# Kernel tuning notes

Measured on AMD Instinct MI355X. Metric: run time of the kernel, lower is better.

The kernel has to match this reference:

```python
import jax, jax.numpy as jnp
from jax import lax
import numpy as np

K, D, BETA = 512, 64, 0.25

def conv1d(x, w, b=None, stride=1, padding=0):
    # x: [N,C,L], w: [O,I,k] (torch layout)
    y = lax.conv_general_dilated(x, w, (stride,), [(padding, padding)],
                                 dimension_numbers=('NCH', 'OIH', 'NCH'))
    return y if b is None else y + b[None, :, None]

def conv_transpose1d(x, w, b, stride, padding):
    # torch ConvTranspose1d; w: [I,O,k]. Equivalent to dilated conv with flipped, transposed kernel.
    k = w.shape[2]
    wf = jnp.flip(w, 2).transpose(1, 0, 2)  # [O,I,k]
    y = lax.conv_general_dilated(x, wf, (1,), [(k - 1 - padding, k - 1 - padding)],
                                 lhs_dilation=(stride,),
                                 dimension_numbers=('NCH', 'OIH', 'NCH'))
    return y + b[None, :, None]

def residual_stack(x, blocks):
    for w1, w2 in blocks:
        h = conv1d(jax.nn.relu(x), w1, None, 1, 1)
        h = conv1d(jax.nn.relu(h), w2, None, 1, 0)
        x = x + h
    return jax.nn.relu(x)

def setup_inputs() -> dict:
    key = jax.random.key(0)
    ks = iter(jax.random.split(key, 32))
    def w(shape, fan_in):
        return jax.random.normal(next(ks), shape, jnp.float32) / np.sqrt(fan_in)
    H, RH = 128, 32
    inp = {
        'x': jax.random.normal(next(ks), (64, 1, 8192), jnp.float32),
        'ec1_w': w((H // 2, 1, 4), 4), 'ec1_b': jnp.zeros(H // 2, jnp.float32),
        'ec2_w': w((H, H // 2, 4), H // 2 * 4), 'ec2_b': jnp.zeros(H, jnp.float32),
        'ec3_w': w((H, H, 3), H * 3), 'ec3_b': jnp.zeros(H, jnp.float32),
        'er1_w1': w((RH, H, 3), H * 3), 'er1_w2': w((H, RH, 1), RH),
        'er2_w1': w((RH, H, 3), H * 3), 'er2_w2': w((H, RH, 1), RH),
        'pvq_w': w((D, H, 1), H), 'pvq_b': jnp.zeros(D, jnp.float32),
        'codebook': jax.random.uniform(next(ks), (K, D), jnp.float32, -1.0 / K, 1.0 / K),
        'dc1_w': w((H, D, 3), D * 3), 'dc1_b': jnp.zeros(H, jnp.float32),
        'dr1_w1': w((RH, H, 3), H * 3), 'dr1_w2': w((H, RH, 1), RH),
        'dr2_w1': w((RH, H, 3), H * 3), 'dr2_w2': w((H, RH, 1), RH),
        'dt1_w': w((H, H // 2, 4), H * 4), 'dt1_b': jnp.zeros(H // 2, jnp.float32),
        'dt2_w': w((H // 2, 1, 4), H // 2 * 4), 'dt2_b': jnp.zeros(1, jnp.float32),
    }
    return inp

def reference(x, ec1_w, ec1_b, ec2_w, ec2_b, ec3_w, ec3_b,
              er1_w1, er1_w2, er2_w1, er2_w2, pvq_w, pvq_b, codebook,
              dc1_w, dc1_b, dr1_w1, dr1_w2, dr2_w1, dr2_w2,
              dt1_w, dt1_b, dt2_w, dt2_b):
    # ---- Encoder (compression_factor == 4) ----
    h = jax.nn.relu(conv1d(x, ec1_w, ec1_b, 2, 1))
    h = jax.nn.relu(conv1d(h, ec2_w, ec2_b, 2, 1))
    h = conv1d(h, ec3_w, ec3_b, 1, 1)
    h = residual_stack(h, [(er1_w1, er1_w2), (er2_w1, er2_w2)])
    z = conv1d(h, pvq_w, pvq_b, 1, 0)            # [B, D, L/4]

    # ---- Vector quantizer ----
    z_blc = z.transpose(0, 2, 1)                 # [B, L', D]
    flat = z_blc.reshape(-1, D)                  # [N, D]
    dists = (jnp.sum(flat * flat, 1, keepdims=True)
             - 2.0 * flat @ codebook.T
             + jnp.sum(codebook * codebook, 1))  # [N, K]
    idx = jnp.argmin(dists, axis=1)              # [N]
    q = codebook[idx].reshape(z_blc.shape)       # [B, L', D]
    e_latent = jnp.mean((lax.stop_gradient(q) - z_blc) ** 2)
    q_latent = jnp.mean((q - lax.stop_gradient(z_blc)) ** 2)
    vq_loss = q_latent + BETA * e_latent
    q_st = z_blc + lax.stop_gradient(q - z_blc)  # straight-through
    counts = jnp.zeros((K,), z.dtype).at[idx].add(1.0)
    avg_probs = counts / idx.shape[0]
    perplexity = jnp.exp(-jnp.sum(avg_probs * jnp.log(avg_probs + 1e-10)))

    # ---- Decoder (compression_factor == 4) ----
    d = conv1d(q_st.transpose(0, 2, 1), dc1_w, dc1_b, 1, 1)
    d = residual_stack(d, [(dr1_w1, dr1_w2), (dr2_w1, dr2_w2)])
    d = jax.nn.relu(conv_transpose1d(d, dt1_w, dt1_b, 2, 1))
    recon = conv_transpose1d(d, dt2_w, dt2_b, 2, 1)  # [B, 1, L]
    return recon, vq_loss, perplexity
```

## Files before the change

### kernel.cpp

```cpp
#include <hip/hip_runtime.h>
#include <math.h>

static constexpr int NB  = 64;
static constexpr int L0  = 8192;
static constexpr int L1  = 4096;
static constexpr int LQ  = 2048;
static constexpr int CH  = 128;
static constexpr int CHH = 64;
static constexpr int CR  = 32;
static constexpr int CD  = 64;
static constexpr int NK  = 512;
static constexpr int NROWS = NB * LQ;

using short8 = __attribute__((ext_vector_type(8))) short;
using f32x4  = __attribute__((ext_vector_type(4))) float;

__device__ inline f32x4 mfma16(short8 a, short8 b, f32x4 c) {
    return __builtin_amdgcn_mfma_f32_16x16x32_bf16(a, b, c, 0, 0, 0);
}

__device__ inline unsigned short bf16rne(float v) {
    unsigned int bb = __builtin_bit_cast(unsigned int, v);
    unsigned int r = (bb + 0x7FFFu + ((bb >> 16) & 1u)) >> 16;
    return (unsigned short)r;
}
__device__ inline float bf2f(unsigned short s) {
    unsigned int u = ((unsigned int)s) << 16;
    return __builtin_bit_cast(float, u);
}

__global__ __launch_bounds__(256) void k_wtf(const float* __restrict__ src,
                                             short* __restrict__ dst,
                                             int CO, int CI, int K, int iok) {
    int i = blockIdx.x * 256 + threadIdx.x;
    int total = K * CO * CI;
    if (i >= total) return;
    int j  = i & 7;
    int hi = (i >> 3) & 3;
    int cl = (i >> 5) & 15;
    int rest = i >> 9;
    int CIb = CI >> 5, COb = CO >> 4;
    int kb = rest % CIb; rest /= CIb;
    int cb = rest % COb;
    int tap = rest / COb;
    int co = cb * 16 + cl, ci = kb * 32 + hi * 8 + j;
    float v = iok ? src[(ci * CO + co) * K + tap] : src[(co * CI + ci) * K + tap];
    dst[i] = (short)bf16rne(v);
}

__global__ __launch_bounds__(256) void k_w2f(const float* __restrict__ src,
                                             short* __restrict__ hi_dst,
                                             short* __restrict__ lo_dst) {
    int i = blockIdx.x * 256 + threadIdx.x;
    if (i >= CH * CR) return;
    int j  = i & 7;
    int hi = (i >> 3) & 3;
    int cl = (i >> 5) & 15;
    int cb = i >> 9;
    int co = cb * 16 + cl, ci = hi * 8 + j;
    float v = src[co * CR + ci];
    unsigned short h = bf16rne(v);
    hi_dst[i] = (short)h;
    lo_dst[i] = (short)bf16rne(v - bf2f(h));
}

__global__ __launch_bounds__(256) void k_pwf(const float* __restrict__ src,
                                             short* __restrict__ hi_dst,
                                             short* __restrict__ lo_dst) {
    int i = blockIdx.x * 256 + threadIdx.x;
    if (i >= CD * CH) return;
    int j  = i & 7;
    int hi = (i >> 3) & 3;
    int cl = (i >> 5) & 15;
    int rest = i >> 9;
    int kb = rest & 3, cb = rest >> 2;
    int d = cb * 16 + cl, ci = kb * 32 + hi * 8 + j;
    float v = src[d * CH + ci];
    unsigned short h = bf16rne(v);
    hi_dst[i] = (short)h;
    lo_dst[i] = (short)bf16rne(v - bf2f(h));
}

__global__ __launch_bounds__(256) void k_cbf(const float* __restrict__ cb,
                                             short* __restrict__ hi_dst,
                                             short* __restrict__ lo_dst) {
    int i = blockIdx.x * 256 + threadIdx.x;
    if (i >= NK * CD) return;
    int j    = i & 7;
    int l    = (i >> 3) & 63;
    int half = (i >> 9) & 1;
    int mt   = i >> 10;
    int cl = l & 15, hi = l >> 4;
    int m = mt * 16 + cl;
    int k = half * 32 + hi * 8 + j;
    float v = -2.f * cb[m * CD + k];
    unsigned short h = bf16rne(v);
    float r = v - bf2f(h);
    hi_dst[i] = (short)h;
    lo_dst[i] = (short)bf16rne(r);
}

__global__ __launch_bounds__(256) void k_ec1(const float* __restrict__ x,
                                             const float* __restrict__ w,
                                             const float* __restrict__ bias,
                                             float* __restrict__ out) {
    int n = blockIdx.x * 256 + threadIdx.x;
    int t  = n & (L1 - 1);
    int co = (n >> 12) & (CHH - 1);
    int b  = n >> 18;
    const float* xp = x + b * L0;
    float acc = bias[co];
    int p0 = 2 * t - 1;
#pragma unroll
    for (int k = 0; k < 4; ++k) {
        int p = p0 + k;
        if (p >= 0 && p < L0) acc += w[co * 4 + k] * xp[p];
    }
    out[n] = fmaxf(acc, 0.f);
}

template <int CIN, int COUT, int NTAPS, int TSTRIDE, int SWS, int LIN,
          bool RELU_IN, bool TRANS_IN, bool HAS_BIAS, bool RELU_OUT>
__global__ __launch_bounds__(256) void k_mfconv2(const float* __restrict__ x,
                                                 const short* __restrict__ wf,
                                                 const float* __restrict__ bias,
                                                 float* __restrict__ out) {
    constexpr int XW = 63 * TSTRIDE + NTAPS;
    constexpr int MR = (COUT == 128) ? 4 : 1;
    constexpr int COb = COUT / 16, CIb = CIN / 32;
    __shared__ unsigned int xsu[CIN * XW / 2];
    int t0 = blockIdx.x * 64;
    int b  = blockIdx.z;
    int tid = threadIdx.x;

    if (TRANS_IN) {
        for (int i = tid; i < XW * (CIN / 2); i += 256) {
            int j = i / (CIN / 2);
            int ci = (i - j * (CIN / 2)) * 2;
            int p = t0 - 1 + j;
            float vx = 0.f, vy = 0.f;
            if (p >= 0 && p < LIN) {
                const float* s = x + ((size_t)b * LIN + p) * CIN + ci;
                vx = s[0]; vy = s[1];
            }
            if (RELU_IN) { vx = fmaxf(vx, 0.f); vy = fmaxf(vy, 0.f); }
            unsigned int u = (__builtin_bit_cast(unsigned int, vx) >> 16)
                           | (__builtin_bit_cast(unsigned int, vy) & 0xFFFF0000u);
            int byte = (j * CIN + ci) * 2;
            byte ^= ((j >> SWS) & 7) << 4;
            xsu[byte >> 2] = u;
        }
    } else {
        for (int i = tid; i < (CIN / 2) * XW; i += 256) {
            int ci2 = i / XW;
            int j = i - ci2 * XW;
            int ci = ci2 * 2;
            int p = t0 * TSTRIDE - 1 + j;
            float vx = 0.f, vy = 0.f;
            if (p >= 0 && p < LIN) {
                const float* s = x + ((size_t)b * CIN + ci) * LIN + p;
                vx = s[0]; vy = s[LIN];
            }
            if (RELU_IN) { vx = fmaxf(vx, 0.f); vy = fmaxf(vy, 0.f); }
            unsigned int u = (__builtin_bit_cast(unsigned int, vx) >> 16)
                           | (__builtin_bit_cast(unsigned int, vy) & 0xFFFF0000u);
            int byte = (j * CIN + ci) * 2;
            byte ^= ((j >> SWS) & 7) << 4;
            xsu[byte >> 2] = u;
        }
    }
    __syncthreads();

    int l  = tid & 63;
    int w  = tid >> 6;
    int cl = l & 15, hi = l >> 4;
    int co_w = (w & 1) * (MR * 16);
    int t_w  = (w >> 1) * 32;

    f32x4 acc[MR][2];
#pragma unroll
    for (int m = 0; m < MR; ++m)
#pragma unroll
        for (int n = 0; n < 2; ++n) acc[m][n] = (f32x4){0.f, 0.f, 0.f, 0.f};

#pragma unroll
    for (int tap = 0; tap < NTAPS; ++tap) {
#pragma unroll
        for (int kb = 0; kb < CIb; ++kb) {
            const short* ap = wf + ((size_t)((tap * COb + co_w / 16) * CIb + kb)) * 512
                            + cl * 32 + hi * 8;
            short8 a[MR];
#pragma unroll
            for (int m = 0; m < MR; ++m)
                a[m] = *reinterpret_cast<const short8*>(ap + (size_t)m * CIb * 512);
            short8 bf[2];
#pragma unroll
            for (int n = 0; n < 2; ++n) {
                int tt = (t_w + n * 16 + cl) * TSTRIDE + tap;
                int byte = (tt * CIN + kb * 32 + hi * 8) * 2;
                byte ^= ((tt >> SWS) & 7) << 4;
                bf[n] = *reinterpret_cast<const short8*>(
                            reinterpret_cast<const char*>(xsu) + byte);
            }
#pragma unroll
            for (int m = 0; m < MR; ++m)
#pragma unroll
                for (int n = 0; n < 2; ++n)
                    acc[m][n] = mfma16(a[m], bf[n], acc[m][n]);
        }
    }

#pragma unroll
    for (int m = 0; m < MR; ++m) {
#pragma unroll
        for (int n = 0; n < 2; ++n) {
#pragma unroll
            for (int r = 0; r < 4; ++r) {
                int co = co_w + m * 16 + hi * 4 + r;
                int t  = t0 + t_w + n * 16 + cl;
                float v = acc[m][n][r];
                if (HAS_BIAS) v += bias[co];
                if (RELU_OUT) v = fmaxf(v, 0.f);
                out[((size_t)b * COUT + co) * LQ + t] = v;
            }
        }
    }
}

__global__ __launch_bounds__(256) void k_dc1g(const int* __restrict__ idx,
                                              const float* __restrict__ cb,
                                              const short* __restrict__ wf,
                                              const float* __restrict__ bias,
                                              float* __restrict__ out) {
    constexpr int XW = 66;
    __shared__ unsigned int xsu[CD * XW / 2];
    int t0 = blockIdx.x * 64;
    int b  = blockIdx.z;
    int tid = threadIdx.x;

    for (int i = tid; i < XW * (CD / 2); i += 256) {
        int j = i >> 5;
        int ci = (i & 31) * 2;
        int p = t0 - 1 + j;
        float vx = 0.f, vy = 0.f;
        if (p >= 0 && p < LQ) {
            int id = idx[(size_t)b * LQ + p];
            const float* s = cb + (size_t)id * CD + ci;
            vx = s[0]; vy = s[1];
        }
        unsigned int u = (__builtin_bit_cast(unsigned int, vx) >> 16)
                       | (__builtin_bit_cast(unsigned int, vy) & 0xFFFF0000u);
        int byte = (j * CD + ci) * 2;
        byte ^= (j & 7) << 4;
        xsu[byte >> 2] = u;
    }
    __syncthreads();

    int l  = tid & 63;
    int w  = tid >> 6;
    int cl = l & 15, hi = l >> 4;
    int co_w = (w & 1) * 64;
    int t_w  = (w >> 1) * 32;

    f32x4 acc[4][2];
#pragma unroll
    for (int m = 0; m < 4; ++m)
#pragma unroll
        for (int n = 0; n < 2; ++n) acc[m][n] = (f32x4){0.f, 0.f, 0.f, 0.f};

#pragma unroll
    for (int tap = 0; tap < 3; ++tap) {
#pragma unroll
        for (int kb = 0; kb < 2; ++kb) {
            const short* ap = wf + ((size_t)((tap * 8 + co_w / 16) * 2 + kb)) * 512
                            + cl * 32 + hi * 8;
            short8 a[4];
#pragma unroll
            for (int m = 0; m < 4; ++m)
                a[m] = *reinterpret_cast<const short8*>(ap + (size_t)m * 2 * 512);
            short8 bf[2];
#pragma unroll
            for (int n = 0; n < 2; ++n) {
                int tt = (t_w + n * 16 + cl) + tap;
                int byte = (tt * CD + kb * 32 + hi * 8) * 2;
                byte ^= (tt & 7) << 4;
                bf[n] = *reinterpret_cast<const short8*>(
                            reinterpret_cast<const char*>(xsu) + byte);
            }
#pragma unroll
            for (int m = 0; m < 4; ++m)
#pragma unroll
                for (int n = 0; n < 2; ++n)
                    acc[m][n] = mfma16(a[m], bf[n], acc[m][n]);
        }
    }

#pragma unroll
    for (int m = 0; m < 4; ++m) {
#pragma unroll
        for (int n = 0; n < 2; ++n) {
#pragma unroll
            for (int r = 0; r < 4; ++r) {
                int co = co_w + m * 16 + hi * 4 + r;
                int t  = t0 + t_w + n * 16 + cl;
                out[((size_t)b * CH + co) * LQ + t] = acc[m][n][r] + bias[co];
            }
        }
    }
}

__global__ __launch_bounds__(256) void k_resblk(const float* __restrict__ src,
                                                float* __restrict__ dst,
                                                const short* __restrict__ wf1,
                                                const short* __restrict__ w2h,
                                                const short* __restrict__ w2l) {
    constexpr int XW = 66;
    __shared__ unsigned int xsu[CH * XW / 2];
    __shared__ unsigned int hh[64 * 16];
    __shared__ unsigned int hl[64 * 16];
    int t0 = blockIdx.x * 64;
    int b  = blockIdx.z;
    int tid = threadIdx.x;

    for (int i = tid; i < (CH / 2) * XW; i += 256) {
        int ci2 = i / XW;
        int j = i - ci2 * XW;
        int ci = ci2 * 2;
        int p = t0 - 1 + j;
        float vx = 0.f, vy = 0.f;
        if (p >= 0 && p < LQ) {
            const float* s = src + ((size_t)b * CH + ci) * LQ + p;
            vx = fmaxf(s[0], 0.f); vy = fmaxf(s[LQ], 0.f);
        }
        unsigned int u = (__builtin_bit_cast(unsigned int, vx) >> 16)
                       | (__builtin_bit_cast(unsigned int, vy) & 0xFFFF0000u);
        int byte = (j * CH + ci) * 2;
        byte ^= (j & 7) << 4;
        xsu[byte >> 2] = u;
    }
    __syncthreads();

    int l  = tid & 63;
    int w  = tid >> 6;
    int cl = l & 15, hi = l >> 4;
    int co_w1 = (w & 1) * 16;
    int t_w   = (w >> 1) * 32;

    f32x4 acc1[2];
    acc1[0] = (f32x4){0.f, 0.f, 0.f, 0.f};
    acc1[1] = (f32x4){0.f, 0.f, 0.f, 0.f};
#pragma unroll
    for (int tap = 0; tap < 3; ++tap) {
#pragma unroll
        for (int kb = 0; kb < 4; ++kb) {
            const short* ap = wf1 + ((size_t)((tap * 2 + (w & 1)) * 4 + kb)) * 512
                            + cl * 32 + hi * 8;
            short8 a = *reinterpret_cast<const short8*>(ap);
#pragma unroll
            for (int n = 0; n < 2; ++n) {
                int tt = (t_w + n * 16 + cl) + tap;
                int byte = (tt * CH + kb * 32 + hi * 8) * 2;
                byte ^= (tt & 7) << 4;
                short8 bf = *reinterpret_cast<const short8*>(
                                reinterpret_cast<const char*>(xsu) + byte);
                acc1[n] = mfma16(a, bf, acc1[n]);
            }
        }
    }

#pragma unroll
    for (int n = 0; n < 2; ++n) {
        int t = t_w + n * 16 + cl;
#pragma unroll
        for (int rp = 0; rp < 2; ++rp) {
            float v0 = fmaxf(acc1[n][2 * rp], 0.f);
            float v1 = fmaxf(acc1[n][2 * rp + 1], 0.f);
            unsigned short h0 = bf16rne(v0), h1 = bf16rne(v1);
            unsigned short l0 = bf16rne(v0 - bf2f(h0)), l1 = bf16rne(v1 - bf2f(h1));
            int ciu = (co_w1 >> 1) + hi * 2 + rp;
            int idx = t * 16 + (ciu ^ ((t & 3) << 2));
            hh[idx] = (unsigned int)h0 | ((unsigned int)h1 << 16);
            hl[idx] = (unsigned int)l0 | ((unsigned int)l1 << 16);
        }
    }
    __syncthreads();

    int co2_w = (w & 1) * 64;
    short8 bh[2], bl[2];
#pragma unroll
    for (int n2 = 0; n2 < 2; ++n2) {
        int t = t_w + n2 * 16 + cl;
        int idx = t * 16 + ((hi * 4) ^ ((t & 3) << 2));
        bh[n2] = *reinterpret_cast<const short8*>(&hh[idx]);
        bl[n2] = *reinterpret_cast<const short8*>(&hl[idx]);
    }
#pragma unroll
    for (int m2 = 0; m2 < 4; ++m2) {
        int co2 = co2_w + m2 * 16;
        const short* aph = w2h + (co2 / 16) * 512 + cl * 32 + hi * 8;
        const short* apl = w2l + (co2 / 16) * 512 + cl * 32 + hi * 8;
        short8 ah = *reinterpret_cast<const short8*>(aph);
        short8 al = *reinterpret_cast<const short8*>(apl);
#pragma unroll
        for (int n2 = 0; n2 < 2; ++n2) {
            f32x4 acc = (f32x4){0.f, 0.f, 0.f, 0.f};
            acc = mfma16(ah, bl[n2], acc);
            acc = mfma16(al, bh[n2], acc);
            acc = mfma16(ah, bh[n2], acc);
            int t = t0 + t_w + n2 * 16 + cl;
#pragma unroll
            for (int r = 0; r < 4; ++r) {
                int co = co2 + hi * 4 + r;
                size_t off = ((size_t)b * CH + co) * LQ + t;
                dst[off] = src[off] + acc[r];
            }
        }
    }
}

__global__ __launch_bounds__(256) void k_dt1m(const float* __restrict__ x,
                                              const short* __restrict__ wf,
                                              const float* __restrict__ bias,
                                              float* __restrict__ out) {
    constexpr int XW = 66;
    __shared__ unsigned int xsu[CH * XW / 2];
    int t0 = blockIdx.x * 64;
    int b  = blockIdx.z;
    int tid = threadIdx.x;
    for (int i = tid; i < (CH / 2) * XW; i += 256) {
        int ci2 = i / XW;
        int j = i - ci2 * XW;
        int ci = ci2 * 2;
        int p = t0 - 1 + j;
        float vx = 0.f, vy = 0.f;
        if (p >= 0 && p < LQ) {
            const float* s = x + ((size_t)b * CH + ci) * LQ + p;
            vx = fmaxf(s[0], 0.f); vy = fmaxf(s[LQ], 0.f);
        }
        unsigned int u = (__builtin_bit_cast(unsigned int, vx) >> 16)
                       | (__builtin_bit_cast(unsigned int, vy) & 0xFFFF0000u);
        int byte = (j * CH + ci) * 2;
        byte ^= (j & 7) << 4;
        xsu[byte >> 2] = u;
    }
    __syncthreads();

    int l  = tid & 63;
    int w  = tid >> 6;
    int cl = l & 15, hi = l >> 4;
    int co_w = (w & 1) * 32;
    int u_w  = (w >> 1) * 32;

    f32x4 ae[2][2], ao[2][2];
#pragma unroll
    for (int m = 0; m < 2; ++m)
#pragma unroll
        for (int n = 0; n < 2; ++n) {
            ae[m][n] = (f32x4){0.f, 0.f, 0.f, 0.f};
            ao[m][n] = (f32x4){0.f, 0.f, 0.f, 0.f};
        }

    const int TK[4] = {1, 3, 0, 2};
    const int TO[4] = {1, 0, 2, 1};
#pragma unroll
    for (int te = 0; te < 4; ++te) {
        int k = TK[te], off = TO[te];
#pragma unroll
        for (int kb = 0; kb < 4; ++kb) {
            const short* ap = wf + (size_t)((k * 4 + co_w / 16) * 4 + kb) * 512
                            + cl * 32 + hi * 8;
            short8 a[2];
#pragma unroll
            for (int m = 0; m < 2; ++m)
                a[m] = *reinterpret_cast<const short8*>(ap + (size_t)m * 4 * 512);
            short8 bf[2];
#pragma unroll
            for (int n = 0; n < 2; ++n) {
                int tt = u_w + n * 16 + cl + off;
                int byte = (tt * CH + kb * 32 + hi * 8) * 2;
                byte ^= (tt & 7) << 4;
                bf[n] = *reinterpret_cast<const short8*>(
                            reinterpret_cast<const char*>(xsu) + byte);
            }
#pragma unroll
            for (int m = 0; m < 2; ++m)
#pragma unroll
                for (int n = 0; n < 2; ++n) {
                    if (te < 2) ae[m][n] = mfma16(a[m], bf[n], ae[m][n]);
                    else        ao[m][n] = mfma16(a[m], bf[n], ao[m][n]);
                }
        }
    }

#pragma unroll
    for (int m = 0; m < 2; ++m) {
#pragma unroll
        for (int n = 0; n < 2; ++n) {
#pragma unroll
            for (int r = 0; r < 4; ++r) {
                int co = co_w + m * 16 + hi * 4 + r;
                int u  = t0 + u_w + n * 16 + cl;
                float bv = bias[co];
                float2 rr;
                rr.x = fmaxf(ae[m][n][r] + bv, 0.f);
                rr.y = fmaxf(ao[m][n][r] + bv, 0.f);
                *reinterpret_cast<float2*>(&out[((size_t)b * CHH + co) * L1 + 2 * u]) = rr;
            }
        }
    }
}

__global__ __launch_bounds__(256) void k_pvqm(const float* __restrict__ x,
                                              const short* __restrict__ pwh,
                                              const short* __restrict__ pwl,
                                              const float* __restrict__ bias,
                                              float* __restrict__ z) {
    __shared__ unsigned int xh[(CH / 2) * 64];
    __shared__ unsigned int xl[(CH / 2) * 64];
    int t0 = blockIdx.x * 64;
    int b  = blockIdx.y;
    int tid = threadIdx.x;

    for (int i = tid; i < (CH / 2) * 64; i += 256) {
        int ci2 = i >> 6;
        int t = i & 63;
        int ci = ci2 * 2;
        const float* s = x + ((size_t)b * CH + ci) * LQ + t0 + t;
        float vx = fmaxf(s[0], 0.f);
        float vy = fmaxf(s[LQ], 0.f);
        unsigned short hx = bf16rne(vx), hy = bf16rne(vy);
        unsigned short lx = bf16rne(vx - bf2f(hx)), ly = bf16rne(vy - bf2f(hy));
        int byte = (t * CH + ci) * 2;
        byte ^= (t & 7) << 4;
        xh[byte >> 2] = (unsigned int)hx | ((unsigned int)hy << 16);
        xl[byte >> 2] = (unsigned int)lx | ((unsigned int)ly << 16);
    }
    __syncthreads();

    int l  = tid & 63;
    int w  = tid >> 6;
    int cl = l & 15, hi = l >> 4;

    float4 bv4 = *reinterpret_cast<const float4*>(&bias[w * 16 + hi * 4]);
    f32x4 acc[4];
#pragma unroll
    for (int nt = 0; nt < 4; ++nt) acc[nt] = (f32x4){bv4.x, bv4.y, bv4.z, bv4.w};

#pragma unroll
    for (int kb = 0; kb < 4; ++kb) {
        const short* aph = pwh + ((size_t)(w * 4 + kb)) * 512 + cl * 32 + hi * 8;
        const short* apl = pwl + ((size_t)(w * 4 + kb)) * 512 + cl * 32 + hi * 8;
        short8 ah = *reinterpret_cast<const short8*>(aph);
        short8 al = *reinterpret_cast<const short8*>(apl);
#pragma unroll
        for (int nt = 0; nt < 4; ++nt) {
            int tt = nt * 16 + cl;
            int byte = (tt * CH + kb * 32 + hi * 8) * 2;
            byte ^= (tt & 7) << 4;
            short8 bhf = *reinterpret_cast<const short8*>(
                             reinterpret_cast<const char*>(xh) + byte);
            short8 blf = *reinterpret_cast<const short8*>(
                             reinterpret_cast<const char*>(xl) + byte);
            acc[nt] = mfma16(ah, blf, acc[nt]);
            acc[nt] = mfma16(al, bhf, acc[nt]);
            acc[nt] = mfma16(ah, bhf, acc[nt]);
        }
    }

#pragma unroll
    for (int nt = 0; nt < 4; ++nt) {
        int t = t0 + nt * 16 + cl;
        float4 o;
        o.x = acc[nt][0]; o.y = acc[nt][1]; o.z = acc[nt][2]; o.w = acc[nt][3];
        *reinterpret_cast<float4*>(&z[((size_t)b * LQ + t) * CD + w * 16 + hi * 4]) = o;
    }
}

__global__ __launch_bounds__(256) void k_cb2(const float* __restrict__ cb,
                                             float* __restrict__ cb2) {
    int k = blockIdx.x * 256 + threadIdx.x;
    if (k >= NK) return;
    const float* r = cb + k * CD;
    float s = 0.f;
#pragma unroll 8
    for (int i = 0; i < CD; ++i) s += r[i] * r[i];
    cb2[k] = s;
}

__global__ __launch_bounds__(256) void k_vqm(const float* __restrict__ z,
                                             const short* __restrict__ cbf_hi,
                                             const short* __restrict__ cbf_lo,
                                             const float* __restrict__ cb2,
                                             const float* __restrict__ cb,
                                             int* __restrict__ idxout,
                                             int* __restrict__ counts,
                                             float* __restrict__ sse) {
    __shared__ float c2l[NK];
    __shared__ int   hist[NK];
    int tid = threadIdx.x;
    int l   = tid & 63;
    int w   = tid >> 6;
    int cl  = l & 15, hi = l >> 4;
    int wrow0 = blockIdx.x * 256 + w * 64;

    for (int i = tid; i < NK; i += 256) { c2l[i] = cb2[i]; hist[i] = 0; }
    __syncthreads();

    short8 bh[4][2], bl[4][2];
#pragma unroll
    for (int nt = 0; nt < 4; ++nt) {
        int row = wrow0 + nt * 16 + cl;
        const float* zr = z + (size_t)row * CD;
#pragma unroll
        for (int half = 0; half < 2; ++half) {
            const float4* p4 = reinterpret_cast<const float4*>(zr + half * 32 + hi * 8);
            float4 v0 = p4[0], v1 = p4[1];
            float vs[8] = {v0.x, v0.y, v0.z, v0.w, v1.x, v1.y, v1.z, v1.w};
            short8 sh, sl;
#pragma unroll
            for (int j = 0; j < 8; ++j) {
                unsigned short h = bf16rne(vs[j]);
                float r = vs[j] - bf2f(h);
                sh[j] = (short)h;
                sl[j] = (short)bf16rne(r);
            }
            bh[nt][half] = sh;
            bl[nt][half] = sl;
        }
    }

    float bscore[4];
    int   bidx[4];
#pragma unroll
    for (int nt = 0; nt < 4; ++nt) { bscore[nt] = 1e30f; bidx[nt] = 0; }

#pragma unroll 4
    for (int mt = 0; mt < 32; ++mt) {
        short8 ah0 = *reinterpret_cast<const short8*>(cbf_hi + (mt * 2 + 0) * 512 + l * 8);
        short8 ah1 = *reinterpret_cast<const short8*>(cbf_hi + (mt * 2 + 1) * 512 + l * 8);
        short8 al0 = *reinterpret_cast<const short8*>(cbf_lo + (mt * 2 + 0) * 512 + l * 8);
        short8 al1 = *reinterpret_cast<const short8*>(cbf_lo + (mt * 2 + 1) * 512 + l * 8);
        float4 c2v = *reinterpret_cast<const float4*>(&c2l[mt * 16 + hi * 4]);
        f32x4 cin = (f32x4){c2v.x, c2v.y, c2v.z, c2v.w};
        int mbase = mt * 16 + hi * 4;
#pragma unroll
        for (int nt = 0; nt < 4; ++nt) {
            f32x4 acc = mfma16(al0, bh[nt][0], cin);
            acc = mfma16(al1, bh[nt][1], acc);
            acc = mfma16(ah0, bl[nt][0], acc);
            acc = mfma16(ah1, bl[nt][1], acc);
            acc = mfma16(ah0, bh[nt][0], acc);
            acc = mfma16(ah1, bh[nt][1], acc);
#pragma unroll
            for (int r = 0; r < 4; ++r) {
                float s = acc[r];
                bool better = s < bscore[nt];
                bscore[nt] = better ? s : bscore[nt];
                bidx[nt]   = better ? (mbase + r) : bidx[nt];
            }
        }
    }

    float err = 0.f;
#pragma unroll
    for (int nt = 0; nt < 4; ++nt) {
        float s = bscore[nt];
        int   id = bidx[nt];
#pragma unroll
        for (int off = 16; off <= 32; off <<= 1) {
            float s2 = __shfl_xor(s, off);
            int   i2 = __shfl_xor(id, off);
            bool take = (s2 < s) || (s2 == s && i2 < id);
            s  = take ? s2 : s;
            id = take ? i2 : id;
        }
        int row = wrow0 + nt * 16 + cl;
        if (hi == 0) idxout[row] = id;
        const float4* cbr = reinterpret_cast<const float4*>(cb + (size_t)id * CD);
        float4 q0 = cbr[hi * 2];
        float4 q1 = cbr[hi * 2 + 1];
        float4 q2 = cbr[8 + hi * 2];
        float4 q3 = cbr[8 + hi * 2 + 1];
        float qv[16] = {q0.x, q0.y, q0.z, q0.w, q1.x, q1.y, q1.z, q1.w,
                        q2.x, q2.y, q2.z, q2.w, q3.x, q3.y, q3.z, q3.w};
#pragma unroll
        for (int half = 0; half < 2; ++half) {
#pragma unroll
            for (int j = 0; j < 8; ++j) {
                float zv = bf2f((unsigned short)bh[nt][half][j])
                         + bf2f((unsigned short)bl[nt][half][j]);
                float d = qv[half * 8 + j] - zv;
                err = fmaf(d, d, err);
            }
        }
        if (hi == 0) atomicAdd(&hist[id], 1);
    }
#pragma unroll
    for (int s = 32; s > 0; s >>= 1) err += __shfl_xor(err, s);
    if (l == 0) atomicAdd(sse, err);

    __syncthreads();
    for (int i = tid; i < NK; i += 256) {
        int h = hist[i];
        if (h) atomicAdd(&counts[i], h);
    }
}

__global__ __launch_bounds__(256) void k_dt2(const float* __restrict__ x,
                                             const float* __restrict__ w,
                                             const float* __restrict__ bias,
                                             float* __restrict__ out) {
    int u = blockIdx.x * 256 + threadIdx.x;
    int b = blockIdx.y;
    const float* xp = x + (size_t)b * CHH * L1 + u;
    float bv = bias[0];
    float ae = bv, ao = bv;
    for (int ci = 0; ci < CHH; ++ci) {
        const float* xr = xp + ci * L1;
        float xm  = (u >= 1) ? xr[-1] : 0.f;
        float x0  = xr[0];
        float xp1 = (u < L1 - 1) ? xr[1] : 0.f;
        const float* wc = w + ci * 4;
        ae += wc[1] * x0 + wc[3] * xm;
        ao += wc[0] * xp1 + wc[2] * x0;
    }
    reinterpret_cast<float2*>(out + (size_t)b * L0)[u] = make_float2(ae, ao);
}

__global__ __launch_bounds__(512) void k_final(const int* __restrict__ counts,
                                               const float* __restrict__ sse,
                                               float* __restrict__ out) {
    __shared__ float red[8];
    int tid = threadIdx.x;
    float p = (float)counts[tid] * (1.f / (float)NROWS);
    float v = p * logf(p + 1e-10f);
#pragma unroll
    for (int s = 32; s > 0; s >>= 1) v += __shfl_down(v, s);
    if ((tid & 63) == 0) red[tid >> 6] = v;
    __syncthreads();
    if (tid == 0) {
        float tot = 0.f;
        for (int i = 0; i < 8; ++i) tot += red[i];
        out[524288] = 1.25f * sse[0] / ((float)NROWS * (float)CD);
        out[524289] = expf(-tot);
    }
}

extern "C" void kernel_launch(void* const* d_in, const int* in_sizes, int n_in,
                              void* d_out, int out_size, void* d_ws, size_t ws_size,
                              hipStream_t stream) {
    const float* x      = (const float*)d_in[0];
    const float* ec1_w  = (const float*)d_in[1];
    const float* ec1_b  = (const float*)d_in[2];
    const float* ec2_w  = (const float*)d_in[3];
    const float* ec2_b  = (const float*)d_in[4];
    const float* ec3_w  = (const float*)d_in[5];
    const float* ec3_b  = (const float*)d_in[6];
    const float* er1_w1 = (const float*)d_in[7];
    const float* er1_w2 = (const float*)d_in[8];
    const float* er2_w1 = (const float*)d_in[9];
    const float* er2_w2 = (const float*)d_in[10];
    const float* pvq_w  = (const float*)d_in[11];
    const float* pvq_b  = (const float*)d_in[12];
    const float* cbk    = (const float*)d_in[13];
    const float* dc1_w  = (const float*)d_in[14];
    const float* dc1_b  = (const float*)d_in[15];
    const float* dr1_w1 = (const float*)d_in[16];
    const float* dr1_w2 = (const float*)d_in[17];
    const float* dr2_w1 = (const float*)d_in[18];
    const float* dr2_w2 = (const float*)d_in[19];
    const float* dt1_w  = (const float*)d_in[20];
    const float* dt1_b  = (const float*)d_in[21];
    const float* dt2_w  = (const float*)d_in[22];
    const float* dt2_b  = (const float*)d_in[23];
    float* out = (float*)d_out;

    char* ws = (char*)d_ws;
    float* A    = (float*)(ws);
    float* Bb   = (float*)(ws + 67108864);
    char*  smal = ws + 134217728;
    int*   counts = (int*)smal;
    float* sse    = (float*)(smal + 2048);
    float* cb2    = (float*)(smal + 4096);
    short* wf_ec2 = (short*)(smal + 8192);
    short* wf_ec3 = wf_ec2 + 32768;
    short* wf_er1 = wf_ec3 + 49152;
    short* wf_er2 = wf_er1 + 12288;
    short* wf_dc1 = wf_er2 + 12288;
    short* wf_dr1 = wf_dc1 + 24576;
    short* wf_dr2 = wf_dr1 + 12288;
    short* wf_dt1 = wf_dr2 + 12288;
    short* cbf_hi = wf_dt1 + 32768;
    short* cbf_lo = cbf_hi + 32768;
    short* w2_er1h = cbf_lo + 32768;
    short* w2_er1l = w2_er1h + 4096;
    short* w2_er2h = w2_er1l + 4096;
    short* w2_er2l = w2_er2h + 4096;
    short* w2_dr1h = w2_er2l + 4096;
    short* w2_dr1l = w2_dr1h + 4096;
    short* w2_dr2h = w2_dr1l + 4096;
    short* w2_dr2l = w2_dr2h + 4096;
    short* pw_hi   = w2_dr2l + 4096;
    short* pw_lo   = pw_hi + 8192;
    float* z = Bb;
    int*   idxv = (int*)((char*)Bb + 33554432);

    hipMemsetAsync(smal, 0, 2056, stream);

    k_wtf<<<dim3(128), 256, 0, stream>>>(ec2_w, wf_ec2, 128, 64, 4, 0);
    k_wtf<<<dim3(192), 256, 0, stream>>>(ec3_w, wf_ec3, 128, 128, 3, 0);
    k_wtf<<<dim3(48), 256, 0, stream>>>(er1_w1, wf_er1, 32, 128, 3, 0);
    k_wtf<<<dim3(48), 256, 0, stream>>>(er2_w1, wf_er2, 32, 128, 3, 0);
    k_wtf<<<dim3(96), 256, 0, stream>>>(dc1_w, wf_dc1, 128, 64, 3, 0);
    k_wtf<<<dim3(48), 256, 0, stream>>>(dr1_w1, wf_dr1, 32, 128, 3, 0);
    k_wtf<<<dim3(48), 256, 0, stream>>>(dr2_w1, wf_dr2, 32, 128, 3, 0);
    k_wtf<<<dim3(128), 256, 0, stream>>>(dt1_w, wf_dt1, 64, 128, 4, 1);
    k_w2f<<<dim3(16), 256, 0, stream>>>(er1_w2, w2_er1h, w2_er1l);
    k_w2f<<<dim3(16), 256, 0, stream>>>(er2_w2, w2_er2h, w2_er2l);
    k_w2f<<<dim3(16), 256, 0, stream>>>(dr1_w2, w2_dr1h, w2_dr1l);
    k_w2f<<<dim3(16), 256, 0, stream>>>(dr2_w2, w2_dr2h, w2_dr2l);
    k_pwf<<<dim3(32), 256, 0, stream>>>(pvq_w, pw_hi, pw_lo);
    k_cbf<<<dim3(128), 256, 0, stream>>>(cbk, cbf_hi, cbf_lo);
    k_cb2<<<dim3(2), 256, 0, stream>>>(cbk, cb2);

    k_ec1<<<dim3((NB * CHH * L1) / 256), 256, 0, stream>>>(x, ec1_w, ec1_b, A);
    k_mfconv2<64, 128, 4, 2, 1, L1, false, false, true, true>
        <<<dim3(LQ / 64, 1, NB), 256, 0, stream>>>(A, wf_ec2, ec2_b, Bb);
    k_mfconv2<128, 128, 3, 1, 0, LQ, false, false, true, false>
        <<<dim3(LQ / 64, 1, NB), 256, 0, stream>>>(Bb, wf_ec3, ec3_b, A);
    k_resblk<<<dim3(LQ / 64, 1, NB), 256, 0, stream>>>(A, Bb, wf_er1, w2_er1h, w2_er1l);
    k_resblk<<<dim3(LQ / 64, 1, NB), 256, 0, stream>>>(Bb, A, wf_er2, w2_er2h, w2_er2l);
    k_pvqm<<<dim3(LQ / 64, NB), 256, 0, stream>>>(A, pw_hi, pw_lo, pvq_b, z);

    k_vqm<<<dim3(NROWS / 256), 256, 0, stream>>>(z, cbf_hi, cbf_lo, cb2, cbk,
                                                 idxv, counts, sse);

    k_dc1g<<<dim3(LQ / 64, 1, NB), 256, 0, stream>>>(idxv, cbk, wf_dc1, dc1_b, A);
    k_resblk<<<dim3(LQ / 64, 1, NB), 256, 0, stream>>>(A, Bb, wf_dr1, w2_dr1h, w2_dr1l);
    k_resblk<<<dim3(LQ / 64, 1, NB), 256, 0, stream>>>(Bb, A, wf_dr2, w2_dr2h, w2_dr2l);
    k_dt1m<<<dim3(LQ / 64, 1, NB), 256, 0, stream>>>(A, wf_dt1, dt1_b, Bb);
    k_dt2<<<dim3(L1 / 256, NB), 256, 0, stream>>>(Bb, dt2_w, dt2_b, out);

    k_final<<<dim3(1), 512, 0, stream>>>(counts, sse, out);
}
```

Measured before the change: 617.8 us.

## Split VQ codebook search across four grid slices with separate reduction kernel

The fused VQ kernel is split in two. The first kernel searches one quarter of the codebook per blockIdx.y and writes a per-row candidate (score, index), which gives four times as many blocks. A second kernel picks the best of the four candidates, writes the index, builds the histogram and accumulates the squared error from fp32 z and the codebook. This adds more parallelism and shortens the serial loop. In exchange, each z row is loaded and split into bf16 four times, there is an extra launch, and a candidate buffer makes an extra round trip through memory.

```diff
diff --git a/kernel.cpp b/kernel.cpp
--- a/kernel.cpp
+++ b/kernel.cpp
@@ -587,24 +587,21 @@
     cb2[k] = s;
 }
 
-__global__ __launch_bounds__(256) void k_vqm(const float* __restrict__ z,
+__global__ __launch_bounds__(256) void k_vqs(const float* __restrict__ z,
                                              const short* __restrict__ cbf_hi,
                                              const short* __restrict__ cbf_lo,
                                              const float* __restrict__ cb2,
-                                             const float* __restrict__ cb,
-                                             int* __restrict__ idxout,
-                                             int* __restrict__ counts,
-                                             float* __restrict__ sse) {
+                                             float2* __restrict__ cand) {
     __shared__ float c2l[NK];
-    __shared__ int   hist[NK];
     int tid = threadIdx.x;
     int l   = tid & 63;
     int w   = tid >> 6;
     int cl  = l & 15, hi = l >> 4;
     int wrow0 = blockIdx.x * 256 + w * 64;
-
-    for (int i = tid; i < NK; i += 256) { c2l[i] = cb2[i]; hist[i] = 0; }
-    __syncthreads();
+    int g = blockIdx.y;
+    int mt0 = g * 8;
+
+    for (int i = tid; i < NK; i += 256) c2l[i] = cb2[i];
 
     short8 bh[4][2], bl[4][2];
 #pragma unroll
@@ -628,14 +625,16 @@
             bl[nt][half] = sl;
         }
     }
+    __syncthreads();
 
     float bscore[4];
     int   bidx[4];
 #pragma unroll
     for (int nt = 0; nt < 4; ++nt) { bscore[nt] = 1e30f; bidx[nt] = 0; }
 
-#pragma unroll 4
-    for (int mt = 0; mt < 32; ++mt) {
+#pragma unroll
+    for (int it = 0; it < 8; ++it) {
+        int mt = mt0 + it;
         short8 ah0 = *reinterpret_cast<const short8*>(cbf_hi + (mt * 2 + 0) * 512 + l * 8);
         short8 ah1 = *reinterpret_cast<const short8*>(cbf_hi + (mt * 2 + 1) * 512 + l * 8);
         short8 al0 = *reinterpret_cast<const short8*>(cbf_lo + (mt * 2 + 0) * 512 + l * 8);
@@ -661,7 +660,6 @@
         }
     }
 
-    float err = 0.f;
 #pragma unroll
     for (int nt = 0; nt < 4; ++nt) {
         float s = bscore[nt];
@@ -674,32 +672,61 @@
             s  = take ? s2 : s;
             id = take ? i2 : id;
         }
-        int row = wrow0 + nt * 16 + cl;
-        if (hi == 0) idxout[row] = id;
-        const float4* cbr = reinterpret_cast<const float4*>(cb + (size_t)id * CD);
-        float4 q0 = cbr[hi * 2];
-        float4 q1 = cbr[hi * 2 + 1];
-        float4 q2 = cbr[8 + hi * 2];
-        float4 q3 = cbr[8 + hi * 2 + 1];
-        float qv[16] = {q0.x, q0.y, q0.z, q0.w, q1.x, q1.y, q1.z, q1.w,
-                        q2.x, q2.y, q2.z, q2.w, q3.x, q3.y, q3.z, q3.w};
-#pragma unroll
-        for (int half = 0; half < 2; ++half) {
-#pragma unroll
-            for (int j = 0; j < 8; ++j) {
-                float zv = bf2f((unsigned short)bh[nt][half][j])
-                         + bf2f((unsigned short)bl[nt][half][j]);
-                float d = qv[half * 8 + j] - zv;
-                err = fmaf(d, d, err);
-            }
-        }
-        if (hi == 0) atomicAdd(&hist[id], 1);
+        if (hi == 0) {
+            int row = wrow0 + nt * 16 + cl;
+            cand[(size_t)row * 4 + g] = make_float2(s, __int_as_float(id));
+        }
+    }
+}
+
+__global__ __launch_bounds__(256) void k_vqr(const float2* __restrict__ cand,
+                                             const float* __restrict__ z,
+                                             const float* __restrict__ cb,
+                                             int* __restrict__ idxout,
+                                             int* __restrict__ counts,
+                                             float* __restrict__ sse) {
+    __shared__ int hist[NK];
+    __shared__ float red[4];
+    int tid = threadIdx.x;
+    int row = blockIdx.x * 256 + tid;
+    for (int i = tid; i < NK; i += 256) hist[i] = 0;
+    __syncthreads();
+
+    const float2* cp = cand + (size_t)row * 4;
+    float2 c0 = cp[0], c1 = cp[1], c2 = cp[2], c3 = cp[3];
+    float bs = c0.x; int bi = __float_as_int(c0.y);
+    {
+        int i1 = __float_as_int(c1.y);
+        bool t1 = (c1.x < bs) || (c1.x == bs && i1 < bi);
+        bs = t1 ? c1.x : bs; bi = t1 ? i1 : bi;
+        int i2 = __float_as_int(c2.y);
+        bool t2 = (c2.x < bs) || (c2.x == bs && i2 < bi);
+        bs = t2 ? c2.x : bs; bi = t2 ? i2 : bi;
+        int i3 = __float_as_int(c3.y);
+        bool t3 = (c3.x < bs) || (c3.x == bs && i3 < bi);
+        bs = t3 ? c3.x : bs; bi = t3 ? i3 : bi;
+    }
+    idxout[row] = bi;
+    atomicAdd(&hist[bi], 1);
+
+    const float4* zr = reinterpret_cast<const float4*>(z + (size_t)row * CD);
+    const float4* cr = reinterpret_cast<const float4*>(cb + (size_t)bi * CD);
+    float err = 0.f;
+#pragma unroll
+    for (int i = 0; i < 16; ++i) {
+        float4 zv = zr[i], cv = cr[i];
+        float dx = cv.x - zv.x, dy = cv.y - zv.y;
+        float dz = cv.z - zv.z, dw = cv.w - zv.w;
+        err += dx * dx + dy * dy + dz * dz + dw * dw;
     }
 #pragma unroll
     for (int s = 32; s > 0; s >>= 1) err += __shfl_xor(err, s);
-    if (l == 0) atomicAdd(sse, err);
-
-    __syncthreads();
+    if ((tid & 63) == 0) red[tid >> 6] = err;
+    __syncthreads();
+    if (tid == 0) {
+        float tot = red[0] + red[1] + red[2] + red[3];
+        atomicAdd(sse, tot);
+    }
     for (int i = tid; i < NK; i += 256) {
         int h = hist[i];
         if (h) atomicAdd(&counts[i], h);
@@ -804,6 +831,7 @@
     short* pw_lo   = pw_hi + 8192;
     float* z = Bb;
     int*   idxv = (int*)((char*)Bb + 33554432);
+    float2* cand = (float2*)((char*)Bb + 34078720);
 
     hipMemsetAsync(smal, 0, 2056, stream);
 
@@ -832,8 +860,8 @@
     k_resblk<<<dim3(LQ / 64, 1, NB), 256, 0, stream>>>(Bb, A, wf_er2, w2_er2h, w2_er2l);
     k_pvqm<<<dim3(LQ / 64, NB), 256, 0, stream>>>(A, pw_hi, pw_lo, pvq_b, z);
 
-    k_vqm<<<dim3(NROWS / 256), 256, 0, stream>>>(z, cbf_hi, cbf_lo, cb2, cbk,
-                                                 idxv, counts, sse);
+    k_vqs<<<dim3(NROWS / 256, 4), 256, 0, stream>>>(z, cbf_hi, cbf_lo, cb2, cand);
+    k_vqr<<<dim3(NROWS / 256), 256, 0, stream>>>(cand, z, cbk, idxv, counts, sse);
 
     k_dc1g<<<dim3(LQ / 64, 1, NB), 256, 0, stream>>>(idxv, cbk, wf_dc1, dc1_b, A);
     k_resblk<<<dim3(LQ / 64, 1, NB), 256, 0, stream>>>(A, Bb, wf_dr1, w2_dr1h, w2_dr1l);
```

Measured after the change: 655.5 us. 1.06x slower.
